# Optimization experiments

Hardware: AMD Instinct MI355X
Metric: run time of the kernel (lower is better)

The kernel has to match this reference:

```python
import jax, jax.numpy as jnp
import numpy as np

NY, NX = 2048, 2048
DX = 5.0
DT = 0.8
BETA = 4.0
RHO = 1.0 / 9.81
EPS_ETA = 0.001
MANNING2 = 0.055 ** 2
PAD = ((0, 0), (0, 0), (1, 1), (1, 1))


def _conv3(x, w):
    # 1-channel 3x3 stencil, VALID padding: [1,1,H+2,W+2] -> [1,1,H,W]
    return jax.lax.conv_general_dilated(
        x, w, window_strides=(1, 1), padding='VALID',
        dimension_numbers=('NCHW', 'OIHW', 'NCHW'))


def _bc_u(u):
    # zero left/right columns, copy top/bottom rows (free-slip in y, no-flow in x)
    p = jnp.pad(u, PAD)
    p = p.at[:, :, 0, :].set(p[:, :, 1, :])
    p = p.at[:, :, -1, :].set(p[:, :, -2, :])
    return p


def _bc_v(v):
    # copy left/right columns, zero top/bottom rows
    p = jnp.pad(v, PAD)
    p = p.at[:, :, :, 0].set(p[:, :, :, 1])
    p = p.at[:, :, :, -1].set(p[:, :, :, -2])
    return p


def _bc_eta(h):
    # Neumann (copy) on all four sides; column copies first, then rows (matches torch order)
    p = jnp.pad(h, PAD)
    p = p.at[:, :, :, -1].set(p[:, :, :, -2])
    p = p.at[:, :, :, 0].set(p[:, :, :, 1])
    p = p.at[:, :, -1, :].set(p[:, :, -2, :])
    p = p.at[:, :, 0, :].set(p[:, :, 1, :])
    return p


def _k_pg(wpad, u, v, w1, w2, w3):
    # Petrov-Galerkin dissipation coefficient
    amp = 0.5 * (jnp.abs(u) + jnp.abs(v)) / DX  # = 1/2 dx^-2 (|u|dx + |v|dx)
    num = 0.25 * DX * jnp.abs(amp * _conv3(wpad, w1))
    den = EPS_ETA + 0.5 * (jnp.abs(_conv3(wpad, w2)) + jnp.abs(_conv3(wpad, w3))) / DX ** 2
    return num / den


def _pg_vector(uu, vv, u, v, k3, w1, w2, w3):
    k_u = _k_pg(uu, u, v, w1, w2, w3)
    k_v = _k_pg(vv, u, v, w1, w2, w3)
    k_uu = jnp.pad(jnp.minimum(k_u, k3), PAD)
    k_vv = jnp.pad(jnp.minimum(k_v, k3), PAD)
    k_x = 0.5 * (k_u * _conv3(uu, w1) + _conv3(uu * k_uu, w1) - u * _conv3(k_uu, w1))
    k_y = 0.5 * (k_v * _conv3(vv, w1) + _conv3(vv * k_vv, w1) - v * _conv3(k_vv, w1))
    return k_x, k_y


def _pg_scalar(hh, h, u, v, k3, w1, w2, w3):
    k_u = _k_pg(hh, u, v, w1, w2, w3)
    k_uu = jnp.pad(jnp.minimum(k_u, k3), PAD)
    return 0.5 * (k_u * _conv3(hh, w1) + _conv3(hh * k_uu, w1) - h * _conv3(k_uu, w1))


def _forward(values_u, values_v, values_H, values_h, k1, k2, k3,
             source_h, dif_values_h, values_hh, w1, w2, w3, wm):
    diag = -w1[0, 0, 1, 1]
    uu = _bc_u(values_u)
    vv = _bc_v(values_v)
    k_x, k_y = _pg_vector(uu, vv, values_u, values_v, k3, w1, w2, w3)
    hp = _bc_eta(values_h)
    # predictor (half) step
    b_u = (k_x * DT - values_u * _conv3(uu, w2) * DT - values_v * _conv3(uu, w3) * DT) * 0.5 + values_u
    b_v = (k_y * DT - values_u * _conv3(vv, w2) * DT - values_v * _conv3(vv, w3) * DT) * 0.5 + values_v
    b_u = b_u - _conv3(hp, w2) * DT
    b_v = b_v - _conv3(hp, w3) * DT
    b_uu = _bc_u(b_u)  # note: padded fields built BEFORE friction division, as in source
    b_vv = _bc_v(b_v)
    depth43 = jnp.maximum(k1, values_H + values_h) ** (4.0 / 3.0)
    sigma_q = jnp.sqrt(b_u ** 2 + b_v ** 2) * MANNING2 / depth43
    b_u = b_u / (1.0 + sigma_q * DT / RHO)
    b_v = b_v / (1.0 + sigma_q * DT / RHO)
    # corrector (full) step
    k_x, k_y = _pg_vector(b_uu, b_vv, b_u, b_v, k3, w1, w2, w3)
    u_n = values_u + k_x * DT - b_u * _conv3(b_uu, w2) * DT - b_v * _conv3(b_uu, w3) * DT
    v_n = values_v + k_y * DT - b_u * _conv3(b_vv, w2) * DT - b_v * _conv3(b_vv, w3) * DT
    u_n = u_n - _conv3(hp, w2) * DT
    v_n = v_n - _conv3(hp, w3) * DT
    sigma_q = jnp.sqrt(u_n ** 2 + v_n ** 2) * MANNING2 / depth43
    u_n = u_n / (1.0 + sigma_q * DT / RHO)
    v_n = v_n / (1.0 + sigma_q * DT / RHO)
    uu = _bc_u(u_n)
    vv = _bc_v(v_n)
    eta1 = jnp.maximum(k2, values_H + values_h)
    eta2 = jnp.maximum(k1, values_H + values_h)
    e1p = _bc_eta(eta1)
    b = BETA * RHO * (
        -_conv3(e1p, w2) * u_n - _conv3(e1p, w3) * v_n
        - eta1 * _conv3(uu, w2) - eta1 * _conv3(vv, w3)
        + _pg_scalar(e1p, eta1, u_n, v_n, k3, w1, w2, w3)
        - _conv3(_bc_eta(dif_values_h), wm) / DT
        + source_h) / (DT * eta2)
    # two Jacobi iterations for the wave (pressure) equation
    coef = BETA * RHO / (DT ** 2 * eta2)
    denom = diag + coef
    hh = values_hh
    for _ in range(2):
        hh = hh - (-_conv3(_bc_eta(hh), w1) + coef * hh) / denom + b / denom
    h_new = values_h + hh
    dif_h = h_new - values_h
    hhp = _bc_eta(hh)
    u_n = u_n - _conv3(hhp, w2) * DT / RHO
    v_n = v_n - _conv3(hhp, w3) * DT / RHO
    return (u_n, v_n, h_new, hh, b, dif_h)


def setup_inputs() -> dict:
    key = jax.random.key(0)
    k = jax.random.split(key, 6)
    shape = (1, 1, NY, NX)
    w1 = jnp.asarray(np.array([[1, 1, 1], [1, -8, 1], [1, 1, 1]], np.float32) / 3.0 / DX ** 2).reshape(1, 1, 3, 3)
    w2 = jnp.asarray(np.array([[-1, 0, 1], [-4, 0, 4], [-1, 0, 1]], np.float32) / 12.0 / DX).reshape(1, 1, 3, 3)
    w3 = jnp.transpose(w2, (0, 1, 3, 2))
    wm = jnp.asarray(np.array([[1, 4, 1], [4, 16, 4], [1, 4, 1]], np.float32) / 36.0).reshape(1, 1, 3, 3)
    return {
        'values_u': jax.random.normal(k[0], shape, jnp.float32) * 0.5,
        'values_v': jax.random.normal(k[1], shape, jnp.float32) * 0.5,
        'values_H': jax.random.uniform(k[2], shape, jnp.float32) * 10.0,  # bathymetric depth
        'values_h': jax.random.normal(k[3], shape, jnp.float32) * 0.1,   # free-surface elevation
        'k1': jnp.full(shape, EPS_ETA, jnp.float32),
        'k2': jnp.zeros(shape, jnp.float32),
        'k3': jnp.full(shape, DX ** 2 * 0.1 / DT, jnp.float32),
        'source_h': jax.random.normal(k[4], shape, jnp.float32) * 0.01,
        'dif_values_h': jax.random.normal(k[5], shape, jnp.float32) * 0.01,
        'values_hh': jnp.zeros(shape, jnp.float32),
        'w1': w1, 'w2': w2, 'w3': w3, 'wm': wm,
    }


def reference(values_u, values_v, values_H, values_h, k1, k2, k3,
              source_h, dif_values_h, values_hh, w1, w2, w3, wm):
    return _forward(values_u, values_v, values_H, values_h, k1, k2, k3,
                    source_h, dif_values_h, values_hh, w1, w2, w3, wm)
```

## Files before the change

### kernel.cpp

```cpp
#include <hip/hip_runtime.h>
#include <math.h>


#define NY 2048
#define NX 2048

#define BX 64
#define BY 8
#define TH (BY + 4)
#define TW (BX + 4)
#define KH (BY + 2)
#define KW (BX + 2)

#define DXf   5.0f
#define DTf   0.8f
#define EPSf  0.001f
#define K3f   3.125f

__device__ constexpr float M2f    = (float)(0.055 * 0.055);
__device__ constexpr float RHO_   = (float)(1.0 / 9.81);
__device__ constexpr float BRf    = (float)(4.0 / 9.81);
__device__ constexpr float DT2f   = (float)(0.8 * 0.8);
__device__ constexpr float C43f   = (float)(4.0 / 3.0);
__device__ constexpr float DTRHO  = 0.8f / RHO_;
__device__ constexpr float INVDT  = 1.0f / 0.8f;
__device__ constexpr float CBRDT2 = BRf / DT2f;

#define W1E ((1.0f / 3.0f) / 25.0f)
#define W1C ((-8.0f / 3.0f) / 25.0f)
#define DIAGf ((8.0f / 3.0f) / 25.0f)
#define W2A ((1.0f / 12.0f) / 5.0f)
#define W2B ((4.0f / 12.0f) / 5.0f)
#define WMA (1.0f / 36.0f)
#define WMB (4.0f / 36.0f)
#define WMC (16.0f / 36.0f)

__device__ __forceinline__ int iclamp(int v, int lo, int hi) {
    return v < lo ? lo : (v > hi ? hi : v);
}

__device__ __forceinline__ float frcp(float x) {
    float r = __builtin_amdgcn_rcpf(x);
    return r * (2.0f - x * r);
}

__device__ __forceinline__ float uuAt(const float* __restrict__ u, int y, int x) {
    if ((unsigned)x >= (unsigned)NX) return 0.0f;
    y = iclamp(y, 0, NY - 1);
    return u[y * NX + x];
}
__device__ __forceinline__ float vvAt(const float* __restrict__ v, int y, int x) {
    if ((unsigned)y >= (unsigned)NY) return 0.0f;
    x = iclamp(x, 0, NX - 1);
    return v[y * NX + x];
}
__device__ __forceinline__ float etaAt(const float* __restrict__ h, int y, int x) {
    y = iclamp(y, 0, NY - 1);
    x = iclamp(x, 0, NX - 1);
    return h[y * NX + x];
}

template<int ST>
__device__ __forceinline__ float cw1f(const float* s) {
    float nb = s[-ST - 1] + s[-ST] + s[-ST + 1] + s[-1] + s[1] + s[ST - 1] + s[ST] + s[ST + 1];
    return W1E * nb + W1C * s[0];
}
template<int ST>
__device__ __forceinline__ float cw2f(const float* s) {
    return W2A * ((s[-ST + 1] - s[-ST - 1]) + (s[ST + 1] - s[ST - 1])) + W2B * (s[1] - s[-1]);
}
template<int ST>
__device__ __forceinline__ float cw3f(const float* s) {
    return W2A * ((s[ST - 1] - s[-ST - 1]) + (s[ST + 1] - s[-ST + 1])) + W2B * (s[ST] - s[-ST]);
}

__device__ __forceinline__ float kpgf(float uq, float vq, float c1, float c2, float c3) {
    float amp = 0.5f * (fabsf(uq) + fabsf(vq)) * 0.2f;
    float num = 1.25f * fabsf(amp * c1);
    float den = EPSf + 0.5f * (fabsf(c2) + fabsf(c3)) * 0.04f;
    return num * frcp(den);
}

template<int FS, int KS>
__device__ __forceinline__ void prod_and_k(const float* pf, const float* pk,
                                           float& prodw1, float& kw1) {
    float k0 = pk[-KS - 1], k1 = pk[-KS], k2 = pk[-KS + 1], k3 = pk[-1], kc = pk[0],
          k4 = pk[1], k5 = pk[KS - 1], k6 = pk[KS], k7 = pk[KS + 1];
    float nbk = k0 + k1 + k2 + k3 + k4 + k5 + k6 + k7;
    float nbp = pf[-FS - 1] * k0 + pf[-FS] * k1 + pf[-FS + 1] * k2 + pf[-1] * k3
              + pf[1] * k4 + pf[FS - 1] * k5 + pf[FS] * k6 + pf[FS + 1] * k7;
    kw1 = W1E * nbk + W1C * kc;
    prodw1 = W1E * nbp + W1C * (pf[0] * kc);
}

__global__ __launch_bounds__(512)
void kA(const float* __restrict__ u, const float* __restrict__ v,
        const float* __restrict__ H, const float* __restrict__ h,
        float* __restrict__ bupre, float* __restrict__ bvpre,
        float* __restrict__ d43o, float* __restrict__ buo, float* __restrict__ bvo)
{
    const int tx0 = blockIdx.x * BX, ty0 = blockIdx.y * BY;
    const int lx = threadIdx.x, ly = threadIdx.y;
    __shared__ float su[TH][TW], sv[TH][TW], sh[KH][KW];
    __shared__ float sku[KH][KW], skum[KH][KW], skv[KH][KW], skvm[KH][KW];
    __shared__ float c1u[KH][KW], c2u[KH][KW], c3u[KH][KW];
    __shared__ float c1v[KH][KW], c2v[KH][KW], c3v[KH][KW];

    for (int r = ly; r < TH; r += BY) {
        int gy = ty0 + r - 2;
        for (int c = lx; c < TW; c += BX) {
            int gx = tx0 + c - 2;
            su[r][c] = uuAt(u, gy, gx);
            sv[r][c] = vvAt(v, gy, gx);
        }
    }
    for (int r = ly; r < KH; r += BY) {
        int gy = ty0 + r - 1;
        for (int c = lx; c < KW; c += BX)
            sh[r][c] = etaAt(h, gy, tx0 + c - 1);
    }
    __syncthreads();

    for (int r = ly; r < KH; r += BY) {
        int gy = ty0 + r - 1;
        for (int c = lx; c < KW; c += BX) {
            int gx = tx0 + c - 1;
            const float* pu = &su[r + 1][c + 1];
            const float* pv = &sv[r + 1][c + 1];
            float a1 = cw1f<TW>(pu), a2 = cw2f<TW>(pu), a3 = cw3f<TW>(pu);
            float b1 = cw1f<TW>(pv), b2 = cw2f<TW>(pv), b3 = cw3f<TW>(pv);
            c1u[r][c] = a1; c2u[r][c] = a2; c3u[r][c] = a3;
            c1v[r][c] = b1; c2v[r][c] = b2; c3v[r][c] = b3;
            float ku = 0.f, kv = 0.f;
            if ((unsigned)gy < (unsigned)NY && (unsigned)gx < (unsigned)NX) {
                float uq = pu[0], vq = pv[0];
                ku = kpgf(uq, vq, a1, a2, a3);
                kv = kpgf(uq, vq, b1, b2, b3);
            }
            sku[r][c] = ku; skum[r][c] = fminf(ku, K3f);
            skv[r][c] = kv; skvm[r][c] = fminf(kv, K3f);
        }
    }
    __syncthreads();

    const int y = ty0 + ly, x = tx0 + lx, idx = y * NX + x;
    const float* pu = &su[ly + 2][lx + 2];
    const float* pv = &sv[ly + 2][lx + 2];
    const float* ph = &sh[ly + 1][lx + 1];
    float uc = pu[0], vc = pv[0];

    float pwu, kwu, pwv, kwv;
    prod_and_k<TW, KW>(pu, &skum[ly + 1][lx + 1], pwu, kwu);
    prod_and_k<TW, KW>(pv, &skvm[ly + 1][lx + 1], pwv, kwv);
    float kx = 0.5f * (sku[ly + 1][lx + 1] * c1u[ly + 1][lx + 1] + pwu - uc * kwu);
    float ky = 0.5f * (skv[ly + 1][lx + 1] * c1v[ly + 1][lx + 1] + pwv - vc * kwv);

    float cw2h = cw2f<KW>(ph), cw3h = cw3f<KW>(ph);

    float bu = (kx * DTf - uc * c2u[ly + 1][lx + 1] * DTf - vc * c3u[ly + 1][lx + 1] * DTf) * 0.5f + uc;
    bu = bu - cw2h * DTf;
    float bv = (ky * DTf - uc * c2v[ly + 1][lx + 1] * DTf - vc * c3v[ly + 1][lx + 1] * DTf) * 0.5f + vc;
    bv = bv - cw3h * DTf;

    float dep = fmaxf(EPSf, H[idx] + ph[0]);
    float d43 = __builtin_amdgcn_exp2f(C43f * __builtin_amdgcn_logf(dep));
    float sq = __builtin_amdgcn_sqrtf(bu * bu + bv * bv) * M2f * frcp(d43);
    float rf = frcp(1.0f + sq * DTRHO);

    bupre[idx] = bu;
    bvpre[idx] = bv;
    d43o[idx] = d43;
    buo[idx] = bu * rf;
    bvo[idx] = bv * rf;
}

__global__ __launch_bounds__(512)
void kB(const float* __restrict__ u, const float* __restrict__ v, const float* __restrict__ h,
        const float* __restrict__ bupre, const float* __restrict__ bvpre,
        const float* __restrict__ bupost, const float* __restrict__ bvpost,
        const float* __restrict__ d43, float* __restrict__ uno, float* __restrict__ vno)
{
    const int tx0 = blockIdx.x * BX, ty0 = blockIdx.y * BY;
    const int lx = threadIdx.x, ly = threadIdx.y;
    __shared__ float su[TH][TW], sv[TH][TW], sh[KH][KW];
    __shared__ float sku[KH][KW], skum[KH][KW], skv[KH][KW], skvm[KH][KW];
    __shared__ float c1u[KH][KW], c2u[KH][KW], c3u[KH][KW];
    __shared__ float c1v[KH][KW], c2v[KH][KW], c3v[KH][KW];

    for (int r = ly; r < TH; r += BY) {
        int gy = ty0 + r - 2;
        for (int c = lx; c < TW; c += BX) {
            int gx = tx0 + c - 2;
            su[r][c] = uuAt(bupre, gy, gx);
            sv[r][c] = vvAt(bvpre, gy, gx);
        }
    }
    for (int r = ly; r < KH; r += BY) {
        int gy = ty0 + r - 1;
        for (int c = lx; c < KW; c += BX)
            sh[r][c] = etaAt(h, gy, tx0 + c - 1);
    }
    __syncthreads();

    for (int r = ly; r < KH; r += BY) {
        int gy = ty0 + r - 1;
        for (int c = lx; c < KW; c += BX) {
            int gx = tx0 + c - 1;
            const float* pu = &su[r + 1][c + 1];
            const float* pv = &sv[r + 1][c + 1];
            float a1 = cw1f<TW>(pu), a2 = cw2f<TW>(pu), a3 = cw3f<TW>(pu);
            float b1 = cw1f<TW>(pv), b2 = cw2f<TW>(pv), b3 = cw3f<TW>(pv);
            c1u[r][c] = a1; c2u[r][c] = a2; c3u[r][c] = a3;
            c1v[r][c] = b1; c2v[r][c] = b2; c3v[r][c] = b3;
            float ku = 0.f, kv = 0.f;
            if ((unsigned)gy < (unsigned)NY && (unsigned)gx < (unsigned)NX) {
                int gi = gy * NX + gx;
                float uq = bupost[gi], vq = bvpost[gi];
                ku = kpgf(uq, vq, a1, a2, a3);
                kv = kpgf(uq, vq, b1, b2, b3);
            }
            sku[r][c] = ku; skum[r][c] = fminf(ku, K3f);
            skv[r][c] = kv; skvm[r][c] = fminf(kv, K3f);
        }
    }
    __syncthreads();

    const int y = ty0 + ly, x = tx0 + lx, idx = y * NX + x;
    const float* pu = &su[ly + 2][lx + 2];
    const float* pv = &sv[ly + 2][lx + 2];
    const float* ph = &sh[ly + 1][lx + 1];
    float buc = bupost[idx], bvc = bvpost[idx];

    float pwu, kwu, pwv, kwv;
    prod_and_k<TW, KW>(pu, &skum[ly + 1][lx + 1], pwu, kwu);
    prod_and_k<TW, KW>(pv, &skvm[ly + 1][lx + 1], pwv, kwv);
    float kx = 0.5f * (sku[ly + 1][lx + 1] * c1u[ly + 1][lx + 1] + pwu - buc * kwu);
    float ky = 0.5f * (skv[ly + 1][lx + 1] * c1v[ly + 1][lx + 1] + pwv - bvc * kwv);

    float un = u[idx] + kx * DTf - buc * c2u[ly + 1][lx + 1] * DTf - bvc * c3u[ly + 1][lx + 1] * DTf;
    un = un - cw2f<KW>(ph) * DTf;
    float vn = v[idx] + ky * DTf - buc * c2v[ly + 1][lx + 1] * DTf - bvc * c3v[ly + 1][lx + 1] * DTf;
    vn = vn - cw3f<KW>(ph) * DTf;

    float sq = __builtin_amdgcn_sqrtf(un * un + vn * vn) * M2f * frcp(d43[idx]);
    float rf = frcp(1.0f + sq * DTRHO);
    uno[idx] = un * rf;
    vno[idx] = vn * rf;
}

__global__ __launch_bounds__(512)
void kC(const float* __restrict__ H, const float* __restrict__ h,
        const float* __restrict__ un, const float* __restrict__ vn,
        const float* __restrict__ dif, const float* __restrict__ src,
        const float* __restrict__ hh0,
        float* __restrict__ bo, float* __restrict__ hh1o)
{
    const int tx0 = blockIdx.x * BX, ty0 = blockIdx.y * BY;
    const int lx = threadIdx.x, ly = threadIdx.y;
    __shared__ float se[TH][TW], sh0[KH][KW];
    __shared__ float sun[KH][KW], svn[KH][KW], sdif[KH][KW];
    __shared__ float sks[KH][KW], sksm[KH][KW];
    __shared__ float c1e[KH][KW], c2e[KH][KW], c3e[KH][KW];

    for (int r = ly; r < TH; r += BY) {
        int gy = ty0 + r - 2;
        for (int c = lx; c < TW; c += BX) {
            int gx = tx0 + c - 2;
            int cy = iclamp(gy, 0, NY - 1), cx = iclamp(gx, 0, NX - 1);
            int gi = cy * NX + cx;
            se[r][c] = fmaxf(0.0f, H[gi] + h[gi]);
        }
    }
    for (int r = ly; r < KH; r += BY) {
        int gy = ty0 + r - 1;
        for (int c = lx; c < KW; c += BX) {
            int gx = tx0 + c - 1;
            sh0[r][c]  = etaAt(hh0, gy, gx);
            sun[r][c]  = uuAt(un, gy, gx);
            svn[r][c]  = vvAt(vn, gy, gx);
            sdif[r][c] = etaAt(dif, gy, gx);
        }
    }
    __syncthreads();

    for (int r = ly; r < KH; r += BY) {
        int gy = ty0 + r - 1;
        for (int c = lx; c < KW; c += BX) {
            int gx = tx0 + c - 1;
            const float* pe = &se[r + 1][c + 1];
            float a1 = cw1f<TW>(pe), a2 = cw2f<TW>(pe), a3 = cw3f<TW>(pe);
            c1e[r][c] = a1; c2e[r][c] = a2; c3e[r][c] = a3;
            float ks = 0.f;
            if ((unsigned)gy < (unsigned)NY && (unsigned)gx < (unsigned)NX)
                ks = kpgf(sun[r][c], svn[r][c], a1, a2, a3);
            sks[r][c] = ks; sksm[r][c] = fminf(ks, K3f);
        }
    }
    __syncthreads();

    const int y = ty0 + ly, x = tx0 + lx, idx = y * NX + x;
    const float* pe = &se[ly + 2][lx + 2];
    float e1c = pe[0];

    float pw, kw;
    prod_and_k<TW, KW>(pe, &sksm[ly + 1][lx + 1], pw, kw);
    float pg = 0.5f * (sks[ly + 1][lx + 1] * c1e[ly + 1][lx + 1] + pw - e1c * kw);

    const float* psu = &sun[ly + 1][lx + 1];
    const float* psv = &svn[ly + 1][lx + 1];
    const float* pd  = &sdif[ly + 1][lx + 1];
    float unc = psu[0], vnc = psv[0];
    float cw2un = cw2f<KW>(psu);
    float cw3vn = cw3f<KW>(psv);
    float cwm = WMA * (pd[-KW - 1] + pd[-KW + 1] + pd[KW - 1] + pd[KW + 1])
              + WMB * (pd[-KW] + pd[-1] + pd[1] + pd[KW])
              + WMC * pd[0];

    float eta2 = fmaxf(EPSf, H[idx] + h[idx]);
    float sum = -c2e[ly + 1][lx + 1] * unc - c3e[ly + 1][lx + 1] * vnc
              - e1c * cw2un - e1c * cw3vn + pg - cwm * INVDT + src[idx];
    float re2 = frcp(eta2);
    float b = (BRf * sum) * INVDT * re2;
    float coef = CBRDT2 * re2;
    float rdn = frcp(DIAGf + coef);

    const float* p0 = &sh0[ly + 1][lx + 1];
    float hc = p0[0];
    float cv = cw1f<KW>(p0);
    float hh1 = hc + (cv - coef * hc) * rdn + b * rdn;

    bo[idx] = b;
    hh1o[idx] = hh1;
}

__global__ __launch_bounds__(512)
void kD(const float* __restrict__ H, const float* __restrict__ h,
        const float* __restrict__ un, const float* __restrict__ vn,
        const float* __restrict__ b, const float* __restrict__ hh1,
        float* __restrict__ o_u, float* __restrict__ o_v, float* __restrict__ o_h,
        float* __restrict__ o_hh, float* __restrict__ o_dif)
{
    const int tx0 = blockIdx.x * BX, ty0 = blockIdx.y * BY;
    const int lx = threadIdx.x, ly = threadIdx.y;
    __shared__ float s1[TH][TW];
    __shared__ float s2[KH][KW];

    for (int r = ly; r < TH; r += BY) {
        int gy = ty0 + r - 2;
        for (int c = lx; c < TW; c += BX)
            s1[r][c] = etaAt(hh1, gy, tx0 + c - 2);
    }
    __syncthreads();

    for (int r = ly; r < KH; r += BY) {
        int cy = iclamp(ty0 + r - 1, 0, NY - 1);
        for (int c = lx; c < KW; c += BX) {
            int cx = iclamp(tx0 + c - 1, 0, NX - 1);
            const float* p = &s1[cy - ty0 + 2][cx - tx0 + 2];
            float hc = p[0];
            float cv = cw1f<TW>(p);
            int gi = cy * NX + cx;
            float coef = CBRDT2 * frcp(fmaxf(EPSf, H[gi] + h[gi]));
            float rdn = frcp(DIAGf + coef);
            s2[r][c] = hc + (cv - coef * hc) * rdn + b[gi] * rdn;
        }
    }
    __syncthreads();

    const int y = ty0 + ly, x = tx0 + lx, idx = y * NX + x;
    const float* p2 = &s2[ly + 1][lx + 1];
    float hh2 = p2[0];
    float hcen = h[idx];
    float hnew = hcen + hh2;

    o_u[idx] = un[idx] - cw2f<KW>(p2) * DTRHO;
    o_v[idx] = vn[idx] - cw3f<KW>(p2) * DTRHO;
    o_h[idx] = hnew;
    o_hh[idx] = hh2;
    o_dif[idx] = hnew - hcen;
}

extern "C" void kernel_launch(void* const* d_in, const int* in_sizes, int n_in,
                              void* d_out, int out_size, void* d_ws, size_t ws_size,
                              hipStream_t stream)
{
    const float* u   = (const float*)d_in[0];
    const float* v   = (const float*)d_in[1];
    const float* H   = (const float*)d_in[2];
    const float* h   = (const float*)d_in[3];
    const float* src = (const float*)d_in[7];
    const float* dif = (const float*)d_in[8];
    const float* hh0 = (const float*)d_in[9];

    float* out = (float*)d_out;
    const size_t N = (size_t)NY * NX;
    float* o0 = out;
    float* o1 = out + N;
    float* o2 = out + 2 * N;
    float* o3 = out + 3 * N;
    float* o4 = out + 4 * N;
    float* o5 = out + 5 * N;

    float* ws  = (float*)d_ws;
    float* un  = ws;
    float* vn  = ws + N;
    float* hh1 = ws + 2 * N;

    dim3 blk(BX, BY);
    dim3 grd(NX / BX, NY / BY);

    kA<<<grd, blk, 0, stream>>>(u, v, H, h, o0, o1, o2, o3, o4);
    kB<<<grd, blk, 0, stream>>>(u, v, h, o0, o1, o3, o4, o2, un, vn);
    kC<<<grd, blk, 0, stream>>>(H, h, un, vn, dif, src, hh0, o4, hh1);
    kD<<<grd, blk, 0, stream>>>(H, h, un, vn, o4, hh1, o0, o1, o2, o3, o5);
}
```

Measured before the change: 460.2 us.

## Replace shared-memory staging with direct global 3x3 loads and interior fast paths

Each kernel now reads stencil neighbourhoods straight from global memory (relying on cache) instead of staging large halo tiles and intermediate conv results in LDS. Interior blocks skip boundary clamping through a templated SAFE flag. kB recomputes d43 instead of reading a stored array, which removes one full-field write and one read. Shared memory shrinks to just the clipped k fields, which should raise occupancy, but convolutions are recomputed and global load counts per thread increase.

Result: faster. 435.5 us (-5.4%).

```diff
diff --git a/kernel.cpp b/kernel.cpp
--- a/kernel.cpp
+++ b/kernel.cpp
@@ -4,13 +4,14 @@
 
 #define NY 2048
 #define NX 2048
-
 #define BX 64
 #define BY 8
+#define GX (NX / BX)
+#define GY (NY / BY)
+#define KH (BY + 2)
+#define KW (BX + 2)
 #define TH (BY + 4)
 #define TW (BX + 4)
-#define KH (BY + 2)
-#define KW (BX + 2)
 
 #define DXf   5.0f
 #define DTf   0.8f
@@ -44,34 +45,56 @@
     return r * (2.0f - x * r);
 }
 
-__device__ __forceinline__ float uuAt(const float* __restrict__ u, int y, int x) {
-    if ((unsigned)x >= (unsigned)NX) return 0.0f;
-    y = iclamp(y, 0, NY - 1);
-    return u[y * NX + x];
-}
-__device__ __forceinline__ float vvAt(const float* __restrict__ v, int y, int x) {
-    if ((unsigned)y >= (unsigned)NY) return 0.0f;
-    x = iclamp(x, 0, NX - 1);
-    return v[y * NX + x];
-}
-__device__ __forceinline__ float etaAt(const float* __restrict__ h, int y, int x) {
-    y = iclamp(y, 0, NY - 1);
-    x = iclamp(x, 0, NX - 1);
-    return h[y * NX + x];
-}
-
-template<int ST>
-__device__ __forceinline__ float cw1f(const float* s) {
-    float nb = s[-ST - 1] + s[-ST] + s[-ST + 1] + s[-1] + s[1] + s[ST - 1] + s[ST] + s[ST + 1];
-    return W1E * nb + W1C * s[0];
-}
-template<int ST>
-__device__ __forceinline__ float cw2f(const float* s) {
-    return W2A * ((s[-ST + 1] - s[-ST - 1]) + (s[ST + 1] - s[ST - 1])) + W2B * (s[1] - s[-1]);
-}
-template<int ST>
-__device__ __forceinline__ float cw3f(const float* s) {
-    return W2A * ((s[ST - 1] - s[-ST - 1]) + (s[ST + 1] - s[-ST + 1])) + W2B * (s[ST] - s[-ST]);
+struct N9 { float m[9]; };
+
+template<bool SAFE, int BC>
+__device__ __forceinline__ float ld(const float* __restrict__ p, int y, int x) {
+    if constexpr (SAFE) {
+        if constexpr (BC == 0) {
+            if ((unsigned)x >= (unsigned)NX) return 0.0f;
+            y = iclamp(y, 0, NY - 1);
+        } else if constexpr (BC == 1) {
+            if ((unsigned)y >= (unsigned)NY) return 0.0f;
+            x = iclamp(x, 0, NX - 1);
+        } else {
+            y = iclamp(y, 0, NY - 1);
+            x = iclamp(x, 0, NX - 1);
+        }
+    }
+    return p[y * NX + x];
+}
+
+template<bool SAFE, int BC>
+__device__ __forceinline__ N9 ld9(const float* __restrict__ p, int y, int x) {
+    N9 n;
+#pragma unroll
+    for (int dy = 0; dy < 3; ++dy)
+#pragma unroll
+        for (int dx = 0; dx < 3; ++dx)
+            n.m[dy * 3 + dx] = ld<SAFE, BC>(p, y + dy - 1, x + dx - 1);
+    return n;
+}
+
+template<int W>
+__device__ __forceinline__ N9 lds9(const float a[][W], int r, int c) {
+    N9 n;
+#pragma unroll
+    for (int dy = 0; dy < 3; ++dy)
+#pragma unroll
+        for (int dx = 0; dx < 3; ++dx)
+            n.m[dy * 3 + dx] = a[r + dy][c + dx];
+    return n;
+}
+
+__device__ __forceinline__ float conv1(const N9& n) {
+    float nb = n.m[0] + n.m[1] + n.m[2] + n.m[3] + n.m[5] + n.m[6] + n.m[7] + n.m[8];
+    return W1E * nb + W1C * n.m[4];
+}
+__device__ __forceinline__ float conv2(const N9& n) {
+    return W2A * ((n.m[2] - n.m[0]) + (n.m[8] - n.m[6])) + W2B * (n.m[5] - n.m[3]);
+}
+__device__ __forceinline__ float conv3(const N9& n) {
+    return W2A * ((n.m[6] - n.m[0]) + (n.m[8] - n.m[2])) + W2B * (n.m[7] - n.m[1]);
 }
 
 __device__ __forceinline__ float kpgf(float uq, float vq, float c1, float c2, float c3) {
@@ -81,124 +104,191 @@
     return num * frcp(den);
 }
 
-template<int FS, int KS>
-__device__ __forceinline__ void prod_and_k(const float* pf, const float* pk,
-                                           float& prodw1, float& kw1) {
-    float k0 = pk[-KS - 1], k1 = pk[-KS], k2 = pk[-KS + 1], k3 = pk[-1], kc = pk[0],
-          k4 = pk[1], k5 = pk[KS - 1], k6 = pk[KS], k7 = pk[KS + 1];
-    float nbk = k0 + k1 + k2 + k3 + k4 + k5 + k6 + k7;
-    float nbp = pf[-FS - 1] * k0 + pf[-FS] * k1 + pf[-FS + 1] * k2 + pf[-1] * k3
-              + pf[1] * k4 + pf[FS - 1] * k5 + pf[FS] * k6 + pf[FS + 1] * k7;
-    kw1 = W1E * nbk + W1C * kc;
-    prodw1 = W1E * nbp + W1C * (pf[0] * kc);
+__device__ __forceinline__ void prodk(const N9& f, const N9& k, float& pw, float& kw) {
+    float nbk = k.m[0] + k.m[1] + k.m[2] + k.m[3] + k.m[5] + k.m[6] + k.m[7] + k.m[8];
+    float nbp = f.m[0] * k.m[0] + f.m[1] * k.m[1] + f.m[2] * k.m[2] + f.m[3] * k.m[3]
+              + f.m[5] * k.m[5] + f.m[6] * k.m[6] + f.m[7] * k.m[7] + f.m[8] * k.m[8];
+    kw = W1E * nbk + W1C * k.m[4];
+    pw = W1E * nbp + W1C * (f.m[4] * k.m[4]);
+}
+
+template<bool SAFE>
+__device__ __forceinline__ void kA_body(
+    const float* __restrict__ u, const float* __restrict__ v,
+    const float* __restrict__ H, const float* __restrict__ h,
+    float* __restrict__ bupre, float* __restrict__ bvpre,
+    float* __restrict__ buo, float* __restrict__ bvo,
+    float (*skum)[KW], float (*skvm)[KW])
+{
+    const int tx0 = blockIdx.x * BX, ty0 = blockIdx.y * BY;
+    const int lx = threadIdx.x, ly = threadIdx.y;
+
+    for (int r = ly; r < KH; r += BY) {
+        int gy = ty0 + r - 1;
+        for (int c = lx; c < KW; c += BX) {
+            int gx = tx0 + c - 1;
+            float kum = 0.f, kvm = 0.f;
+            if (!SAFE || ((unsigned)gy < (unsigned)NY && (unsigned)gx < (unsigned)NX)) {
+                N9 fu = ld9<SAFE, 0>(u, gy, gx);
+                N9 fv = ld9<SAFE, 1>(v, gy, gx);
+                float uq = fu.m[4], vq = fv.m[4];
+                float ku = kpgf(uq, vq, conv1(fu), conv2(fu), conv3(fu));
+                float kv = kpgf(uq, vq, conv1(fv), conv2(fv), conv3(fv));
+                kum = fminf(ku, K3f);
+                kvm = fminf(kv, K3f);
+            }
+            skum[r][c] = kum;
+            skvm[r][c] = kvm;
+        }
+    }
+    __syncthreads();
+
+    const int y = ty0 + ly, x = tx0 + lx, idx = y * NX + x;
+    N9 fu = ld9<SAFE, 0>(u, y, x);
+    N9 fv = ld9<SAFE, 1>(v, y, x);
+    N9 fh = ld9<SAFE, 2>(h, y, x);
+    float uc = fu.m[4], vc = fv.m[4];
+    float c1u = conv1(fu), c2u = conv2(fu), c3u = conv3(fu);
+    float c1v = conv1(fv), c2v = conv2(fv), c3v = conv3(fv);
+    float sku = kpgf(uc, vc, c1u, c2u, c3u);
+    float skv = kpgf(uc, vc, c1v, c2v, c3v);
+
+    N9 k9u = lds9<KW>(skum, ly, lx);
+    N9 k9v = lds9<KW>(skvm, ly, lx);
+    float pwu, kwu, pwv, kwv;
+    prodk(fu, k9u, pwu, kwu);
+    prodk(fv, k9v, pwv, kwv);
+    float kx = 0.5f * (sku * c1u + pwu - uc * kwu);
+    float ky = 0.5f * (skv * c1v + pwv - vc * kwv);
+
+    float bu = (kx * DTf - uc * c2u * DTf - vc * c3u * DTf) * 0.5f + uc;
+    bu = bu - conv2(fh) * DTf;
+    float bv = (ky * DTf - uc * c2v * DTf - vc * c3v * DTf) * 0.5f + vc;
+    bv = bv - conv3(fh) * DTf;
+
+    float dep = fmaxf(EPSf, H[idx] + fh.m[4]);
+    float d43 = __builtin_amdgcn_exp2f(C43f * __builtin_amdgcn_logf(dep));
+    float sq = __builtin_amdgcn_sqrtf(bu * bu + bv * bv) * M2f * frcp(d43);
+    float rf = frcp(1.0f + sq * DTRHO);
+
+    bupre[idx] = bu;
+    bvpre[idx] = bv;
+    buo[idx] = bu * rf;
+    bvo[idx] = bv * rf;
 }
 
 __global__ __launch_bounds__(512)
 void kA(const float* __restrict__ u, const float* __restrict__ v,
         const float* __restrict__ H, const float* __restrict__ h,
         float* __restrict__ bupre, float* __restrict__ bvpre,
-        float* __restrict__ d43o, float* __restrict__ buo, float* __restrict__ bvo)
+        float* __restrict__ buo, float* __restrict__ bvo)
+{
+    __shared__ float skum[KH][KW], skvm[KH][KW];
+    const bool safe = blockIdx.x == 0 || blockIdx.x == GX - 1 ||
+                      blockIdx.y == 0 || blockIdx.y == GY - 1;
+    if (safe) kA_body<true >(u, v, H, h, bupre, bvpre, buo, bvo, skum, skvm);
+    else      kA_body<false>(u, v, H, h, bupre, bvpre, buo, bvo, skum, skvm);
+}
+
+template<bool SAFE>
+__device__ __forceinline__ void kB_body(
+    const float* __restrict__ u, const float* __restrict__ v,
+    const float* __restrict__ h, const float* __restrict__ H,
+    const float* __restrict__ bupre, const float* __restrict__ bvpre,
+    const float* __restrict__ bupost, const float* __restrict__ bvpost,
+    float* __restrict__ uno, float* __restrict__ vno,
+    float (*skum)[KW], float (*skvm)[KW])
 {
     const int tx0 = blockIdx.x * BX, ty0 = blockIdx.y * BY;
     const int lx = threadIdx.x, ly = threadIdx.y;
-    __shared__ float su[TH][TW], sv[TH][TW], sh[KH][KW];
-    __shared__ float sku[KH][KW], skum[KH][KW], skv[KH][KW], skvm[KH][KW];
-    __shared__ float c1u[KH][KW], c2u[KH][KW], c3u[KH][KW];
-    __shared__ float c1v[KH][KW], c2v[KH][KW], c3v[KH][KW];
-
-    for (int r = ly; r < TH; r += BY) {
-        int gy = ty0 + r - 2;
-        for (int c = lx; c < TW; c += BX) {
-            int gx = tx0 + c - 2;
-            su[r][c] = uuAt(u, gy, gx);
-            sv[r][c] = vvAt(v, gy, gx);
-        }
-    }
-    for (int r = ly; r < KH; r += BY) {
-        int gy = ty0 + r - 1;
-        for (int c = lx; c < KW; c += BX)
-            sh[r][c] = etaAt(h, gy, tx0 + c - 1);
-    }
-    __syncthreads();
 
     for (int r = ly; r < KH; r += BY) {
         int gy = ty0 + r - 1;
         for (int c = lx; c < KW; c += BX) {
             int gx = tx0 + c - 1;
-            const float* pu = &su[r + 1][c + 1];
-            const float* pv = &sv[r + 1][c + 1];
-            float a1 = cw1f<TW>(pu), a2 = cw2f<TW>(pu), a3 = cw3f<TW>(pu);
-            float b1 = cw1f<TW>(pv), b2 = cw2f<TW>(pv), b3 = cw3f<TW>(pv);
-            c1u[r][c] = a1; c2u[r][c] = a2; c3u[r][c] = a3;
-            c1v[r][c] = b1; c2v[r][c] = b2; c3v[r][c] = b3;
-            float ku = 0.f, kv = 0.f;
-            if ((unsigned)gy < (unsigned)NY && (unsigned)gx < (unsigned)NX) {
-                float uq = pu[0], vq = pv[0];
-                ku = kpgf(uq, vq, a1, a2, a3);
-                kv = kpgf(uq, vq, b1, b2, b3);
+            float kum = 0.f, kvm = 0.f;
+            if (!SAFE || ((unsigned)gy < (unsigned)NY && (unsigned)gx < (unsigned)NX)) {
+                N9 fu = ld9<SAFE, 0>(bupre, gy, gx);
+                N9 fv = ld9<SAFE, 1>(bvpre, gy, gx);
+                int gi = gy * NX + gx;
+                float uq = bupost[gi], vq = bvpost[gi];
+                float ku = kpgf(uq, vq, conv1(fu), conv2(fu), conv3(fu));
+                float kv = kpgf(uq, vq, conv1(fv), conv2(fv), conv3(fv));
+                kum = fminf(ku, K3f);
+                kvm = fminf(kv, K3f);
             }
-            sku[r][c] = ku; skum[r][c] = fminf(ku, K3f);
-            skv[r][c] = kv; skvm[r][c] = fminf(kv, K3f);
+            skum[r][c] = kum;
+            skvm[r][c] = kvm;
         }
     }
     __syncthreads();
 
     const int y = ty0 + ly, x = tx0 + lx, idx = y * NX + x;
-    const float* pu = &su[ly + 2][lx + 2];
-    const float* pv = &sv[ly + 2][lx + 2];
-    const float* ph = &sh[ly + 1][lx + 1];
-    float uc = pu[0], vc = pv[0];
-
+    N9 fu = ld9<SAFE, 0>(bupre, y, x);
+    N9 fv = ld9<SAFE, 1>(bvpre, y, x);
+    N9 fh = ld9<SAFE, 2>(h, y, x);
+    float buc = bupost[idx], bvc = bvpost[idx];
+    float c1u = conv1(fu), c2u = conv2(fu), c3u = conv3(fu);
+    float c1v = conv1(fv), c2v = conv2(fv), c3v = conv3(fv);
+    float sku = kpgf(buc, bvc, c1u, c2u, c3u);
+    float skv = kpgf(buc, bvc, c1v, c2v, c3v);
+
+    N9 k9u = lds9<KW>(skum, ly, lx);
+    N9 k9v = lds9<KW>(skvm, ly, lx);
     float pwu, kwu, pwv, kwv;
-    prod_and_k<TW, KW>(pu, &skum[ly + 1][lx + 1], pwu, kwu);
-    prod_and_k<TW, KW>(pv, &skvm[ly + 1][lx + 1], pwv, kwv);
-    float kx = 0.5f * (sku[ly + 1][lx + 1] * c1u[ly + 1][lx + 1] + pwu - uc * kwu);
-    float ky = 0.5f * (skv[ly + 1][lx + 1] * c1v[ly + 1][lx + 1] + pwv - vc * kwv);
-
-    float cw2h = cw2f<KW>(ph), cw3h = cw3f<KW>(ph);
-
-    float bu = (kx * DTf - uc * c2u[ly + 1][lx + 1] * DTf - vc * c3u[ly + 1][lx + 1] * DTf) * 0.5f + uc;
-    bu = bu - cw2h * DTf;
-    float bv = (ky * DTf - uc * c2v[ly + 1][lx + 1] * DTf - vc * c3v[ly + 1][lx + 1] * DTf) * 0.5f + vc;
-    bv = bv - cw3h * DTf;
-
-    float dep = fmaxf(EPSf, H[idx] + ph[0]);
+    prodk(fu, k9u, pwu, kwu);
+    prodk(fv, k9v, pwv, kwv);
+    float kx = 0.5f * (sku * c1u + pwu - buc * kwu);
+    float ky = 0.5f * (skv * c1v + pwv - bvc * kwv);
+
+    float un = u[idx] + kx * DTf - buc * c2u * DTf - bvc * c3u * DTf;
+    un = un - conv2(fh) * DTf;
+    float vn = v[idx] + ky * DTf - buc * c2v * DTf - bvc * c3v * DTf;
+    vn = vn - conv3(fh) * DTf;
+
+    float dep = fmaxf(EPSf, H[idx] + fh.m[4]);
     float d43 = __builtin_amdgcn_exp2f(C43f * __builtin_amdgcn_logf(dep));
-    float sq = __builtin_amdgcn_sqrtf(bu * bu + bv * bv) * M2f * frcp(d43);
+    float sq = __builtin_amdgcn_sqrtf(un * un + vn * vn) * M2f * frcp(d43);
     float rf = frcp(1.0f + sq * DTRHO);
-
-    bupre[idx] = bu;
-    bvpre[idx] = bv;
-    d43o[idx] = d43;
-    buo[idx] = bu * rf;
-    bvo[idx] = bv * rf;
+    uno[idx] = un * rf;
+    vno[idx] = vn * rf;
 }
 
 __global__ __launch_bounds__(512)
-void kB(const float* __restrict__ u, const float* __restrict__ v, const float* __restrict__ h,
+void kB(const float* __restrict__ u, const float* __restrict__ v,
+        const float* __restrict__ h, const float* __restrict__ H,
         const float* __restrict__ bupre, const float* __restrict__ bvpre,
         const float* __restrict__ bupost, const float* __restrict__ bvpost,
-        const float* __restrict__ d43, float* __restrict__ uno, float* __restrict__ vno)
+        float* __restrict__ uno, float* __restrict__ vno)
+{
+    __shared__ float skum[KH][KW], skvm[KH][KW];
+    const bool safe = blockIdx.x == 0 || blockIdx.x == GX - 1 ||
+                      blockIdx.y == 0 || blockIdx.y == GY - 1;
+    if (safe) kB_body<true >(u, v, h, H, bupre, bvpre, bupost, bvpost, uno, vno, skum, skvm);
+    else      kB_body<false>(u, v, h, H, bupre, bvpre, bupost, bvpost, uno, vno, skum, skvm);
+}
+
+template<bool SAFE>
+__device__ __forceinline__ void kC_body(
+    const float* __restrict__ H, const float* __restrict__ h,
+    const float* __restrict__ un, const float* __restrict__ vn,
+    const float* __restrict__ dif, const float* __restrict__ src,
+    const float* __restrict__ hh0,
+    float* __restrict__ bo, float* __restrict__ hh1o,
+    float (*se)[TW], float (*sksm)[KW])
 {
     const int tx0 = blockIdx.x * BX, ty0 = blockIdx.y * BY;
     const int lx = threadIdx.x, ly = threadIdx.y;
-    __shared__ float su[TH][TW], sv[TH][TW], sh[KH][KW];
-    __shared__ float sku[KH][KW], skum[KH][KW], skv[KH][KW], skvm[KH][KW];
-    __shared__ float c1u[KH][KW], c2u[KH][KW], c3u[KH][KW];
-    __shared__ float c1v[KH][KW], c2v[KH][KW], c3v[KH][KW];
 
     for (int r = ly; r < TH; r += BY) {
-        int gy = ty0 + r - 2;
+        int cy = ty0 + r - 2;
+        if (SAFE) cy = iclamp(cy, 0, NY - 1);
         for (int c = lx; c < TW; c += BX) {
-            int gx = tx0 + c - 2;
-            su[r][c] = uuAt(bupre, gy, gx);
-            sv[r][c] = vvAt(bvpre, gy, gx);
-        }
-    }
-    for (int r = ly; r < KH; r += BY) {
-        int gy = ty0 + r - 1;
-        for (int c = lx; c < KW; c += BX)
-            sh[r][c] = etaAt(h, gy, tx0 + c - 1);
+            int cx = tx0 + c - 2;
+            if (SAFE) cx = iclamp(cx, 0, NX - 1);
+            int gi = cy * NX + cx;
+            se[r][c] = fmaxf(0.0f, H[gi] + h[gi]);
+        }
     }
     __syncthreads();
 
@@ -206,46 +296,55 @@
         int gy = ty0 + r - 1;
         for (int c = lx; c < KW; c += BX) {
             int gx = tx0 + c - 1;
-            const float* pu = &su[r + 1][c + 1];
-            const float* pv = &sv[r + 1][c + 1];
-            float a1 = cw1f<TW>(pu), a2 = cw2f<TW>(pu), a3 = cw3f<TW>(pu);
-            float b1 = cw1f<TW>(pv), b2 = cw2f<TW>(pv), b3 = cw3f<TW>(pv);
-            c1u[r][c] = a1; c2u[r][c] = a2; c3u[r][c] = a3;
-            c1v[r][c] = b1; c2v[r][c] = b2; c3v[r][c] = b3;
-            float ku = 0.f, kv = 0.f;
-            if ((unsigned)gy < (unsigned)NY && (unsigned)gx < (unsigned)NX) {
+            float ksm = 0.f;
+            if (!SAFE || ((unsigned)gy < (unsigned)NY && (unsigned)gx < (unsigned)NX)) {
+                N9 fe = lds9<TW>(se, r, c);
                 int gi = gy * NX + gx;
-                float uq = bupost[gi], vq = bvpost[gi];
-                ku = kpgf(uq, vq, a1, a2, a3);
-                kv = kpgf(uq, vq, b1, b2, b3);
+                float ks = kpgf(un[gi], vn[gi], conv1(fe), conv2(fe), conv3(fe));
+                ksm = fminf(ks, K3f);
             }
-            sku[r][c] = ku; skum[r][c] = fminf(ku, K3f);
-            skv[r][c] = kv; skvm[r][c] = fminf(kv, K3f);
+            sksm[r][c] = ksm;
         }
     }
     __syncthreads();
 
     const int y = ty0 + ly, x = tx0 + lx, idx = y * NX + x;
-    const float* pu = &su[ly + 2][lx + 2];
-    const float* pv = &sv[ly + 2][lx + 2];
-    const float* ph = &sh[ly + 1][lx + 1];
-    float buc = bupost[idx], bvc = bvpost[idx];
-
-    float pwu, kwu, pwv, kwv;
-    prod_and_k<TW, KW>(pu, &skum[ly + 1][lx + 1], pwu, kwu);
-    prod_and_k<TW, KW>(pv, &skvm[ly + 1][lx + 1], pwv, kwv);
-    float kx = 0.5f * (sku[ly + 1][lx + 1] * c1u[ly + 1][lx + 1] + pwu - buc * kwu);
-    float ky = 0.5f * (skv[ly + 1][lx + 1] * c1v[ly + 1][lx + 1] + pwv - bvc * kwv);
-
-    float un = u[idx] + kx * DTf - buc * c2u[ly + 1][lx + 1] * DTf - bvc * c3u[ly + 1][lx + 1] * DTf;
-    un = un - cw2f<KW>(ph) * DTf;
-    float vn = v[idx] + ky * DTf - buc * c2v[ly + 1][lx + 1] * DTf - bvc * c3v[ly + 1][lx + 1] * DTf;
-    vn = vn - cw3f<KW>(ph) * DTf;
-
-    float sq = __builtin_amdgcn_sqrtf(un * un + vn * vn) * M2f * frcp(d43[idx]);
-    float rf = frcp(1.0f + sq * DTRHO);
-    uno[idx] = un * rf;
-    vno[idx] = vn * rf;
+    N9 fe = lds9<TW>(se, ly + 1, lx + 1);
+    float e1c = fe.m[4];
+    float c1e = conv1(fe), c2e = conv2(fe), c3e = conv3(fe);
+
+    N9 fun = ld9<SAFE, 0>(un, y, x);
+    N9 fvn = ld9<SAFE, 1>(vn, y, x);
+    float unc = fun.m[4], vnc = fvn.m[4];
+    float sks = kpgf(unc, vnc, c1e, c2e, c3e);
+
+    N9 k9 = lds9<KW>(sksm, ly, lx);
+    float pw, kw;
+    prodk(fe, k9, pw, kw);
+    float pg = 0.5f * (sks * c1e + pw - e1c * kw);
+
+    float cw2un = conv2(fun);
+    float cw3vn = conv3(fvn);
+    N9 fd = ld9<SAFE, 2>(dif, y, x);
+    float cwm = WMA * (fd.m[0] + fd.m[2] + fd.m[6] + fd.m[8])
+              + WMB * (fd.m[1] + fd.m[3] + fd.m[5] + fd.m[7])
+              + WMC * fd.m[4];
+
+    float eta2 = fmaxf(EPSf, e1c);
+    float sum = -c2e * unc - c3e * vnc - e1c * cw2un - e1c * cw3vn + pg
+              - cwm * INVDT + src[idx];
+    float re2 = frcp(eta2);
+    float b = (BRf * sum) * INVDT * re2;
+    float coef = CBRDT2 * re2;
+    float rdn = frcp(DIAGf + coef);
+
+    N9 f0 = ld9<SAFE, 2>(hh0, y, x);
+    float hc = f0.m[4];
+    float cv = conv1(f0);
+    float hh1 = hc + (cv - coef * hc) * rdn + b * rdn;
+
+    bo[idx] = b;
+    hh1o[idx] = hh1;
 }
 
 __global__ __launch_bounds__(512)
@@ -255,82 +354,54 @@
         const float* __restrict__ hh0,
         float* __restrict__ bo, float* __restrict__ hh1o)
 {
+    __shared__ float se[TH][TW];
+    __shared__ float sksm[KH][KW];
+    const bool safe = blockIdx.x == 0 || blockIdx.x == GX - 1 ||
+                      blockIdx.y == 0 || blockIdx.y == GY - 1;
+    if (safe) kC_body<true >(H, h, un, vn, dif, src, hh0, bo, hh1o, se, sksm);
+    else      kC_body<false>(H, h, un, vn, dif, src, hh0, bo, hh1o, se, sksm);
+}
+
+template<bool SAFE>
+__device__ __forceinline__ void kD_body(
+    const float* __restrict__ H, const float* __restrict__ h,
+    const float* __restrict__ un, const float* __restrict__ vn,
+    const float* __restrict__ b, const float* __restrict__ hh1,
+    float* __restrict__ o_u, float* __restrict__ o_v, float* __restrict__ o_h,
+    float* __restrict__ o_hh, float* __restrict__ o_dif,
+    float (*s2)[KW])
+{
     const int tx0 = blockIdx.x * BX, ty0 = blockIdx.y * BY;
     const int lx = threadIdx.x, ly = threadIdx.y;
-    __shared__ float se[TH][TW], sh0[KH][KW];
-    __shared__ float sun[KH][KW], svn[KH][KW], sdif[KH][KW];
-    __shared__ float sks[KH][KW], sksm[KH][KW];
-    __shared__ float c1e[KH][KW], c2e[KH][KW], c3e[KH][KW];
-
-    for (int r = ly; r < TH; r += BY) {
-        int gy = ty0 + r - 2;
-        for (int c = lx; c < TW; c += BX) {
-            int gx = tx0 + c - 2;
-            int cy = iclamp(gy, 0, NY - 1), cx = iclamp(gx, 0, NX - 1);
+
+    for (int r = ly; r < KH; r += BY) {
+        int cy = ty0 + r - 1;
+        if (SAFE) cy = iclamp(cy, 0, NY - 1);
+        for (int c = lx; c < KW; c += BX) {
+            int cx = tx0 + c - 1;
+            if (SAFE) cx = iclamp(cx, 0, NX - 1);
+            N9 f1 = ld9<SAFE, 2>(hh1, cy, cx);
+            float hc = f1.m[4];
+            float cv = conv1(f1);
             int gi = cy * NX + cx;
-            se[r][c] = fmaxf(0.0f, H[gi] + h[gi]);
-        }
-    }
-    for (int r = ly; r < KH; r += BY) {
-        int gy = ty0 + r - 1;
-        for (int c = lx; c < KW; c += BX) {
-            int gx = tx0 + c - 1;
-            sh0[r][c]  = etaAt(hh0, gy, gx);
-            sun[r][c]  = uuAt(un, gy, gx);
-            svn[r][c]  = vvAt(vn, gy, gx);
-            sdif[r][c] = etaAt(dif, gy, gx);
+            float coef = CBRDT2 * frcp(fmaxf(EPSf, H[gi] + h[gi]));
+            float rdn = frcp(DIAGf + coef);
+            s2[r][c] = hc + (cv - coef * hc) * rdn + b[gi] * rdn;
         }
     }
     __syncthreads();
 
-    for (int r = ly; r < KH; r += BY) {
-        int gy = ty0 + r - 1;
-        for (int c = lx; c < KW; c += BX) {
-            int gx = tx0 + c - 1;
-            const float* pe = &se[r + 1][c + 1];
-            float a1 = cw1f<TW>(pe), a2 = cw2f<TW>(pe), a3 = cw3f<TW>(pe);
-            c1e[r][c] = a1; c2e[r][c] = a2; c3e[r][c] = a3;
-            float ks = 0.f;
-            if ((unsigned)gy < (unsigned)NY && (unsigned)gx < (unsigned)NX)
-                ks = kpgf(sun[r][c], svn[r][c], a1, a2, a3);
-            sks[r][c] = ks; sksm[r][c] = fminf(ks, K3f);
-        }
-    }
-    __syncthreads();
-
     const int y = ty0 + ly, x = tx0 + lx, idx = y * NX + x;
-    const float* pe = &se[ly + 2][lx + 2];
-    float e1c = pe[0];
-
-    float pw, kw;
-    prod_and_k<TW, KW>(pe, &sksm[ly + 1][lx + 1], pw, kw);
-    float pg = 0.5f * (sks[ly + 1][lx + 1] * c1e[ly + 1][lx + 1] + pw - e1c * kw);
-
-    const float* psu = &sun[ly + 1][lx + 1];
-    const float* psv = &svn[ly + 1][lx + 1];
-    const float* pd  = &sdif[ly + 1][lx + 1];
-    float unc = psu[0], vnc = psv[0];
-    float cw2un = cw2f<KW>(psu);
-    float cw3vn = cw3f<KW>(psv);
-    float cwm = WMA * (pd[-KW - 1] + pd[-KW + 1] + pd[KW - 1] + pd[KW + 1])
-              + WMB * (pd[-KW] + pd[-1] + pd[1] + pd[KW])
-              + WMC * pd[0];
-
-    float eta2 = fmaxf(EPSf, H[idx] + h[idx]);
-    float sum = -c2e[ly + 1][lx + 1] * unc - c3e[ly + 1][lx + 1] * vnc
-              - e1c * cw2un - e1c * cw3vn + pg - cwm * INVDT + src[idx];
-    float re2 = frcp(eta2);
-    float b = (BRf * sum) * INVDT * re2;
-    float coef = CBRDT2 * re2;
-    float rdn = frcp(DIAGf + coef);
-
-    const float* p0 = &sh0[ly + 1][lx + 1];
-    float hc = p0[0];
-    float cv = cw1f<KW>(p0);
-    float hh1 = hc + (cv - coef * hc) * rdn + b * rdn;
-
-    bo[idx] = b;
-    hh1o[idx] = hh1;
+    N9 p2 = lds9<KW>(s2, ly, lx);
+    float hh2 = p2.m[4];
+    float hcen = h[idx];
+    float hnew = hcen + hh2;
+
+    o_u[idx] = un[idx] - conv2(p2) * DTRHO;
+    o_v[idx] = vn[idx] - conv3(p2) * DTRHO;
+    o_h[idx] = hnew;
+    o_hh[idx] = hh2;
+    o_dif[idx] = hnew - hcen;
 }
 
 __global__ __launch_bounds__(512)
@@ -340,44 +411,11 @@
         float* __restrict__ o_u, float* __restrict__ o_v, float* __restrict__ o_h,
         float* __restrict__ o_hh, float* __restrict__ o_dif)
 {
-    const int tx0 = blockIdx.x * BX, ty0 = blockIdx.y * BY;
-    const int lx = threadIdx.x, ly = threadIdx.y;
-    __shared__ float s1[TH][TW];
     __shared__ float s2[KH][KW];
-
-    for (int r = ly; r < TH; r += BY) {
-        int gy = ty0 + r - 2;
-        for (int c = lx; c < TW; c += BX)
-            s1[r][c] = etaAt(hh1, gy, tx0 + c - 2);
-    }
-    __syncthreads();
-
-    for (int r = ly; r < KH; r += BY) {
-        int cy = iclamp(ty0 + r - 1, 0, NY - 1);
-        for (int c = lx; c < KW; c += BX) {
-            int cx = iclamp(tx0 + c - 1, 0, NX - 1);
-            const float* p = &s1[cy - ty0 + 2][cx - tx0 + 2];
-            float hc = p[0];
-            float cv = cw1f<TW>(p);
-            int gi = cy * NX + cx;
-            float coef = CBRDT2 * frcp(fmaxf(EPSf, H[gi] + h[gi]));
-            float rdn = frcp(DIAGf + coef);
-            s2[r][c] = hc + (cv - coef * hc) * rdn + b[gi] * rdn;
-        }
-    }
-    __syncthreads();
-
-    const int y = ty0 + ly, x = tx0 + lx, idx = y * NX + x;
-    const float* p2 = &s2[ly + 1][lx + 1];
-    float hh2 = p2[0];
-    float hcen = h[idx];
-    float hnew = hcen + hh2;
-
-    o_u[idx] = un[idx] - cw2f<KW>(p2) * DTRHO;
-    o_v[idx] = vn[idx] - cw3f<KW>(p2) * DTRHO;
-    o_h[idx] = hnew;
-    o_hh[idx] = hh2;
-    o_dif[idx] = hnew - hcen;
+    const bool safe = blockIdx.x == 0 || blockIdx.x == GX - 1 ||
+                      blockIdx.y == 0 || blockIdx.y == GY - 1;
+    if (safe) kD_body<true >(H, h, un, vn, b, hh1, o_u, o_v, o_h, o_hh, o_dif, s2);
+    else      kD_body<false>(H, h, un, vn, b, hh1, o_u, o_v, o_h, o_hh, o_dif, s2);
 }
 
 extern "C" void kernel_launch(void* const* d_in, const int* in_sizes, int n_in,
@@ -407,10 +445,10 @@
     float* hh1 = ws + 2 * N;
 
     dim3 blk(BX, BY);
-    dim3 grd(NX / BX, NY / BY);
-
-    kA<<<grd, blk, 0, stream>>>(u, v, H, h, o0, o1, o2, o3, o4);
-    kB<<<grd, blk, 0, stream>>>(u, v, h, o0, o1, o3, o4, o2, un, vn);
+    dim3 grd(GX, GY);
+
+    kA<<<grd, blk, 0, stream>>>(u, v, H, h, o0, o1, o3, o4);
+    kB<<<grd, blk, 0, stream>>>(u, v, h, H, o0, o1, o3, o4, un, vn);
     kC<<<grd, blk, 0, stream>>>(H, h, un, vn, dif, src, hh0, o4, hh1);
     kD<<<grd, blk, 0, stream>>>(H, h, un, vn, o4, hh1, o0, o1, o2, o3, o5);
 }
```
